# Kernel tuning notes

Measured on AMD Instinct MI355X. Metric: run time of the kernel, lower is better.

## Reference

```python
import jax, jax.numpy as jnp
import numpy as np

N = 40000      # nodes
E = 640000     # edges (avg degree 16)
F_IN = 32      # input node feature dim
G = 64         # graphs in batch
DIMS = [(F_IN, 128), (128, 64), (64, 32), (32, 16)]


def setup_inputs() -> dict:
    key = jax.random.key(0)
    ks = jax.random.split(key, 16)
    inp = {
        "x": jax.random.normal(ks[0], (N, F_IN), jnp.float32),
        "edge_index": jax.random.randint(ks[1], (2, E), 0, N),
        "batch": jnp.sort(jax.random.randint(ks[2], (N,), 0, G)),
    }
    k = 3
    for i, (din, dout) in enumerate(DIMS, 1):
        s = 1.0 / np.sqrt(din)
        inp[f"W{i}_rel"] = jax.random.uniform(ks[k], (din, dout), jnp.float32, -s, s); k += 1
        inp[f"b{i}"] = jax.random.uniform(ks[k], (dout,), jnp.float32, -s, s); k += 1
        inp[f"W{i}_root"] = jax.random.uniform(ks[k], (din, dout), jnp.float32, -s, s); k += 1
    s = 1.0 / np.sqrt(16)
    inp["Wfc"] = jax.random.uniform(ks[15], (16, 1), jnp.float32, -s, s)
    inp["bfc"] = jax.random.uniform(jax.random.fold_in(key, 99), (1,), jnp.float32, -s, s)
    return inp


def _graph_conv(x, src, dst, W_rel, b, W_root):
    # PyG GraphConv (aggr='add'): out_i = (sum_{j->i} x_j) @ W_rel + b + x_i @ W_root
    agg = jax.ops.segment_sum(x[src], dst, num_segments=N)  # gather -> scatter-add
    return agg @ W_rel + b + x @ W_root


def reference(x, edge_index, batch,
              W1_rel, b1, W1_root, W2_rel, b2, W2_root,
              W3_rel, b3, W3_root, W4_rel, b4, W4_root, Wfc, bfc):
    src, dst = edge_index[0], edge_index[1]
    h = jax.nn.relu(_graph_conv(x, src, dst, W1_rel, b1, W1_root))
    h = jax.nn.relu(_graph_conv(h, src, dst, W2_rel, b2, W2_root))
    h = jax.nn.relu(_graph_conv(h, src, dst, W3_rel, b3, W3_root))
    h = _graph_conv(h, src, dst, W4_rel, b4, W4_root)  # no ReLU before pooling
    # global mean pool per graph
    sums = jax.ops.segment_sum(h, batch, num_segments=G)                       # [G, 16]
    counts = jax.ops.segment_sum(jnp.ones((N, 1), h.dtype), batch, num_segments=G)
    pooled = sums / jnp.maximum(counts, 1.0)
    return pooled @ Wfc + bfc  # [G, 1]
```

## Files before the change

kernel.cpp:

```cpp
#include <hip/hip_runtime.h>

#define NN 40000
#define NE 640000
#define NG 64
#define SCAN_NB ((NN + 255) / 256)
#define CCAP 768

__device__ __forceinline__ float fcomp(const float4& v, int t) {
    return t == 0 ? v.x : t == 1 ? v.y : t == 2 ? v.z : v.w;
}
__device__ __forceinline__ unsigned int pack2bf(float a, float b) {
    unsigned int ua = __float_as_uint(a);
    unsigned int ub = __float_as_uint(b);
    ua = (ua + 0x7fffu + ((ua >> 16) & 1u)) >> 16;
    ub = (ub + 0x7fffu + ((ub >> 16) & 1u)) >> 16;
    return ua | (ub << 16);
}
__device__ __forceinline__ uint2 pack4bf(const float4& v) {
    return make_uint2(pack2bf(v.x, v.y), pack2bf(v.z, v.w));
}
__device__ __forceinline__ float lo2f(unsigned int u) { return __uint_as_float(u << 16); }
__device__ __forceinline__ float hi2f(unsigned int u) { return __uint_as_float(u & 0xffff0000u); }
__device__ __forceinline__ void acc8(const uint4& u, float4& lo, float4& hi) {
    lo.x += lo2f(u.x); lo.y += hi2f(u.x); lo.z += lo2f(u.y); lo.w += hi2f(u.y);
    hi.x += lo2f(u.z); hi.y += hi2f(u.z); hi.z += lo2f(u.w); hi.w += hi2f(u.w);
}

__global__ __launch_bounds__(256) void prep_kernel(
        int* __restrict__ zp, int nz,
        const float4* __restrict__ x4,
        uint2* __restrict__ xb,
        const float* __restrict__ W4rel,
        const float* __restrict__ W4root,
        const float* __restrict__ b4,
        const float* __restrict__ Wfc,
        float* __restrict__ wf) {
    int i = blockIdx.x * 256 + threadIdx.x;
    if (i < nz) zp[i] = 0;
    if (i < NN * 8) { float4 v = x4[i]; xb[i] = pack4bf(v); }
    if (blockIdx.x == 0) {
        int t = threadIdx.x;
        if (t < 32) {
            float a = 0.f, b = 0.f;
#pragma unroll
            for (int j = 0; j < 16; ++j) {
                float w = Wfc[j];
                a += W4rel[t * 16 + j] * w;
                b += W4root[t * 16 + j] * w;
            }
            wf[t] = a;
            wf[32 + t] = b;
        } else if (t == 32) {
            float s = 0.f;
#pragma unroll
            for (int j = 0; j < 16; ++j) s += b4[j] * Wfc[j];
            wf[64] = s;
        }
    }
}

__global__ void hist_kernel(const int* __restrict__ dst, int* __restrict__ deg,
                            int* __restrict__ epos) {
    int e = blockIdx.x * blockDim.x + threadIdx.x;
    if (e < NE) epos[e] = atomicAdd(&deg[dst[e]], 1);
}

__global__ __launch_bounds__(256) void scan1_kernel(const int* __restrict__ deg,
                                                    int* __restrict__ rowptr,
                                                    int* __restrict__ bsum) {
    __shared__ int ws[4];
    __shared__ int wpre[4];
    int i = blockIdx.x * 256 + threadIdx.x;
    int lane = threadIdx.x & 63, wid = threadIdx.x >> 6;
    int v = (i < NN) ? deg[i] : 0;
    int incl = v;
#pragma unroll
    for (int off = 1; off < 64; off <<= 1) {
        int u = __shfl_up(incl, off, 64);
        if (lane >= off) incl += u;
    }
    if (lane == 63) ws[wid] = incl;
    __syncthreads();
    if (threadIdx.x == 0) {
        int s = 0;
#pragma unroll
        for (int w = 0; w < 4; ++w) { wpre[w] = s; s += ws[w]; }
        bsum[blockIdx.x] = s;
    }
    __syncthreads();
    if (i < NN) rowptr[i] = wpre[wid] + (incl - v);
}

__global__ __launch_bounds__(256) void scan23_kernel(int* __restrict__ rowptr,
                                                     const int* __restrict__ bsum) {
    __shared__ int ws[4];
    int t = threadIdx.x, b = blockIdx.x;
    int v = (t < b) ? bsum[t] : 0;
#pragma unroll
    for (int off = 32; off; off >>= 1) v += __shfl_xor(v, off, 64);
    if ((t & 63) == 0) ws[t >> 6] = v;
    __syncthreads();
    int soff = ws[0] + ws[1] + ws[2] + ws[3];
    int i = b * 256 + t;
    if (i < NN) rowptr[i] += soff;
    if (b == SCAN_NB - 1 && t == 0) rowptr[NN] = soff + bsum[b];
}

__global__ void fill_kernel(const int* __restrict__ src, const int* __restrict__ dst,
                            const int* __restrict__ rowptr, const int* __restrict__ epos,
                            int* __restrict__ col) {
    int e = blockIdx.x * blockDim.x + threadIdx.x;
    if (e < NE) col[rowptr[dst[e]] + epos[e]] = src[e];
}

__global__ __launch_bounds__(256, 4) void fconv1_kernel(
        const uint4* __restrict__ xb4,
        const float4* __restrict__ x,
        const int* __restrict__ rowptr,
        const int* __restrict__ col,
        const float4* __restrict__ Wrel,
        const float4* __restrict__ Wroot,
        const float4* __restrict__ bias,
        float4* __restrict__ out) {
    __shared__ float4 sA[32][9];
    __shared__ float4 sR[32 * 32];
    __shared__ float4 sT[32 * 32];
    __shared__ int scol[CCAP];
    int t = threadIdx.x;
    for (int i = t; i < 32 * 32; i += 256) { sR[i] = Wrel[i]; sT[i] = Wroot[i]; }
    int blk0 = blockIdx.x * 32;
    int ebeg = rowptr[blk0], eend = rowptr[blk0 + 32];
    bool gat = t < 128;
    int na = t >> 2, c = t & 3;
    int node = blk0 + (gat ? na : 0);
    int beg = gat ? rowptr[node] : 0;
    int end = gat ? rowptr[node + 1] : 0;
    float4 aLo = {0.f, 0.f, 0.f, 0.f}, aHi = {0.f, 0.f, 0.f, 0.f};
    for (int base = ebeg; base < eend; base += CCAP) {
        int cnt = eend - base < CCAP ? eend - base : CCAP;
        __syncthreads();
        for (int i = t; i < cnt; i += 256) scol[i] = col[base + i];
        __syncthreads();
        if (gat) {
            int lo = beg > base ? beg : base;
            int hi = end < base + cnt ? end : base + cnt;
            int e = lo;
            for (; e + 4 <= hi; e += 4) {
                uint4 u0 = xb4[(size_t)scol[e - base] * 4 + c];
                uint4 u1 = xb4[(size_t)scol[e - base + 1] * 4 + c];
                uint4 u2 = xb4[(size_t)scol[e - base + 2] * 4 + c];
                uint4 u3 = xb4[(size_t)scol[e - base + 3] * 4 + c];
                acc8(u0, aLo, aHi); acc8(u1, aLo, aHi);
                acc8(u2, aLo, aHi); acc8(u3, aLo, aHi);
            }
            for (; e < hi; ++e) {
                uint4 u = xb4[(size_t)scol[e - base] * 4 + c];
                acc8(u, aLo, aHi);
            }
        }
    }
    if (gat) { sA[na][2 * c] = aLo; sA[na][2 * c + 1] = aHi; }
    __syncthreads();
    int jg = t % 16, mg = t / 16;
    int n0 = blk0 + mg * 2;
    float4 bb0 = bias[2 * jg], bb1 = bias[2 * jg + 1];
    float4 acc00 = bb0, acc01 = bb1, acc10 = bb0, acc11 = bb1;
#pragma unroll 2
    for (int kc = 0; kc < 8; ++kc) {
        float4 a0 = sA[2 * mg][kc];
        float4 a1 = sA[2 * mg + 1][kc];
        float4 x0 = x[(size_t)n0 * 8 + kc];
        float4 x1 = x[(size_t)(n0 + 1) * 8 + kc];
#pragma unroll
        for (int tt = 0; tt < 4; ++tt) {
            int k = kc * 4 + tt;
            float4 wr0 = sR[k * 32 + 2 * jg], wr1 = sR[k * 32 + 2 * jg + 1];
            float4 wt0 = sT[k * 32 + 2 * jg], wt1 = sT[k * 32 + 2 * jg + 1];
            float av0 = fcomp(a0, tt), xv0 = fcomp(x0, tt);
            float av1 = fcomp(a1, tt), xv1 = fcomp(x1, tt);
            acc00.x += av0 * wr0.x + xv0 * wt0.x;
            acc00.y += av0 * wr0.y + xv0 * wt0.y;
            acc00.z += av0 * wr0.z + xv0 * wt0.z;
            acc00.w += av0 * wr0.w + xv0 * wt0.w;
            acc01.x += av0 * wr1.x + xv0 * wt1.x;
            acc01.y += av0 * wr1.y + xv0 * wt1.y;
            acc01.z += av0 * wr1.z + xv0 * wt1.z;
            acc01.w += av0 * wr1.w + xv0 * wt1.w;
            acc10.x += av1 * wr0.x + xv1 * wt0.x;
            acc10.y += av1 * wr0.y + xv1 * wt0.y;
            acc10.z += av1 * wr0.z + xv1 * wt0.z;
            acc10.w += av1 * wr0.w + xv1 * wt0.w;
            acc11.x += av1 * wr1.x + xv1 * wt1.x;
            acc11.y += av1 * wr1.y + xv1 * wt1.y;
            acc11.z += av1 * wr1.z + xv1 * wt1.z;
            acc11.w += av1 * wr1.w + xv1 * wt1.w;
        }
    }
    float4 r;
    r.x = fmaxf(acc00.x, 0.f); r.y = fmaxf(acc00.y, 0.f);
    r.z = fmaxf(acc00.z, 0.f); r.w = fmaxf(acc00.w, 0.f);
    out[(size_t)n0 * 32 + 2 * jg] = r;
    r.x = fmaxf(acc01.x, 0.f); r.y = fmaxf(acc01.y, 0.f);
    r.z = fmaxf(acc01.z, 0.f); r.w = fmaxf(acc01.w, 0.f);
    out[(size_t)n0 * 32 + 2 * jg + 1] = r;
    r.x = fmaxf(acc10.x, 0.f); r.y = fmaxf(acc10.y, 0.f);
    r.z = fmaxf(acc10.z, 0.f); r.w = fmaxf(acc10.w, 0.f);
    out[(size_t)(n0 + 1) * 32 + 2 * jg] = r;
    r.x = fmaxf(acc11.x, 0.f); r.y = fmaxf(acc11.y, 0.f);
    r.z = fmaxf(acc11.z, 0.f); r.w = fmaxf(acc11.w, 0.f);
    out[(size_t)(n0 + 1) * 32 + 2 * jg + 1] = r;
}

__global__ __launch_bounds__(256, 6) void mmyz_kernel(
        const float4* __restrict__ h,
        const float4* __restrict__ Wrel,
        const float4* __restrict__ Wroot,
        const float4* __restrict__ bias,
        uint2* __restrict__ y2b,
        float4* __restrict__ z2) {
    __shared__ float4 sR[32 * 16];
    __shared__ float4 sT[32 * 16];
    int jl = threadIdx.x % 16;
    int mg = threadIdx.x / 16;
    int n0 = blockIdx.x * 32 + mg * 2;
    float4 bb = bias[jl];
    float4 ay0 = {0.f, 0.f, 0.f, 0.f}, ay1 = {0.f, 0.f, 0.f, 0.f};
    float4 az0 = bb, az1 = bb;
    for (int s = 0; s < 4; ++s) {
        if (s) __syncthreads();
        for (int i = threadIdx.x; i < 512; i += 256) {
            sR[i] = Wrel[s * 512 + i];
            sT[i] = Wroot[s * 512 + i];
        }
        __syncthreads();
#pragma unroll 2
        for (int kc = 0; kc < 8; ++kc) {
            float4 h0 = h[(size_t)n0 * 32 + s * 8 + kc];
            float4 h1 = h[(size_t)(n0 + 1) * 32 + s * 8 + kc];
#pragma unroll
            for (int tt = 0; tt < 4; ++tt) {
                float4 wr = sR[(kc * 4 + tt) * 16 + jl];
                float4 wt = sT[(kc * 4 + tt) * 16 + jl];
                float v0 = fcomp(h0, tt), v1 = fcomp(h1, tt);
                ay0.x += v0 * wr.x; ay0.y += v0 * wr.y;
                ay0.z += v0 * wr.z; ay0.w += v0 * wr.w;
                az0.x += v0 * wt.x; az0.y += v0 * wt.y;
                az0.z += v0 * wt.z; az0.w += v0 * wt.w;
                ay1.x += v1 * wr.x; ay1.y += v1 * wr.y;
                ay1.z += v1 * wr.z; ay1.w += v1 * wr.w;
                az1.x += v1 * wt.x; az1.y += v1 * wt.y;
                az1.z += v1 * wt.z; az1.w += v1 * wt.w;
            }
        }
    }
    y2b[(size_t)n0 * 16 + jl] = pack4bf(ay0);
    z2[(size_t)n0 * 16 + jl] = az0;
    y2b[(size_t)(n0 + 1) * 16 + jl] = pack4bf(ay1);
    z2[(size_t)(n0 + 1) * 16 + jl] = az1;
}

__global__ __launch_bounds__(256, 5) void fconv3_kernel(
        const uint4* __restrict__ yb4,
        const float4* __restrict__ z,
        const int* __restrict__ rowptr,
        const int* __restrict__ col,
        const float4* __restrict__ Wrel,
        const float4* __restrict__ Wroot,
        const float4* __restrict__ bias,
        uint2* __restrict__ y3b,
        float4* __restrict__ z3) {
    __shared__ float4 sH[32][17];
    __shared__ float4 sR[64 * 8];
    __shared__ float4 sT[64 * 8];
    __shared__ int scol[CCAP];
    int t = threadIdx.x;
    for (int i = t; i < 64 * 8; i += 256) { sR[i] = Wrel[i]; sT[i] = Wroot[i]; }
    int blk0 = blockIdx.x * 32;
    int ebeg = rowptr[blk0], eend = rowptr[blk0 + 32];
    int na = t >> 3, c = t & 7;
    int node = blk0 + na;
    int beg = rowptr[node], end = rowptr[node + 1];
    float4 aLo = z[(size_t)node * 16 + 2 * c];
    float4 aHi = z[(size_t)node * 16 + 2 * c + 1];
    for (int base = ebeg; base < eend; base += CCAP) {
        int cnt = eend - base < CCAP ? eend - base : CCAP;
        __syncthreads();
        for (int i = t; i < cnt; i += 256) scol[i] = col[base + i];
        __syncthreads();
        int lo = beg > base ? beg : base;
        int hi = end < base + cnt ? end : base + cnt;
        int e = lo;
        for (; e + 4 <= hi; e += 4) {
            uint4 u0 = yb4[(size_t)scol[e - base] * 8 + c];
            uint4 u1 = yb4[(size_t)scol[e - base + 1] * 8 + c];
            uint4 u2 = yb4[(size_t)scol[e - base + 2] * 8 + c];
            uint4 u3 = yb4[(size_t)scol[e - base + 3] * 8 + c];
            acc8(u0, aLo, aHi); acc8(u1, aLo, aHi);
            acc8(u2, aLo, aHi); acc8(u3, aLo, aHi);
        }
        for (; e < hi; ++e) {
            uint4 u = yb4[(size_t)scol[e - base] * 8 + c];
            acc8(u, aLo, aHi);
        }
    }
    aLo.x = fmaxf(aLo.x, 0.f); aLo.y = fmaxf(aLo.y, 0.f);
    aLo.z = fmaxf(aLo.z, 0.f); aLo.w = fmaxf(aLo.w, 0.f);
    aHi.x = fmaxf(aHi.x, 0.f); aHi.y = fmaxf(aHi.y, 0.f);
    aHi.z = fmaxf(aHi.z, 0.f); aHi.w = fmaxf(aHi.w, 0.f);
    sH[na][2 * c] = aLo;
    sH[na][2 * c + 1] = aHi;
    __syncthreads();
    int jl = t & 7, mg = t >> 3;
    int nodeB = blk0 + mg;
    float4 ay = {0.f, 0.f, 0.f, 0.f};
    float4 az = bias[jl];
#pragma unroll 4
    for (int kc = 0; kc < 16; ++kc) {
        float4 h4 = sH[mg][kc];
#pragma unroll
        for (int tt = 0; tt < 4; ++tt) {
            float hv = fcomp(h4, tt);
            float4 wr = sR[(kc * 4 + tt) * 8 + jl];
            float4 wt = sT[(kc * 4 + tt) * 8 + jl];
            ay.x += hv * wr.x; ay.y += hv * wr.y;
            ay.z += hv * wr.z; ay.w += hv * wr.w;
            az.x += hv * wt.x; az.y += hv * wt.y;
            az.z += hv * wt.z; az.w += hv * wt.w;
        }
    }
    y3b[(size_t)nodeB * 8 + jl] = pack4bf(ay);
    z3[(size_t)nodeB * 8 + jl] = az;
}

__global__ __launch_bounds__(256, 8) void fconv4_kernel(
        const uint4* __restrict__ yb4,
        const float4* __restrict__ z,
        const int* __restrict__ rowptr,
        const int* __restrict__ col,
        const float* __restrict__ wf,
        float* __restrict__ y4,
        float* __restrict__ z4) {
    __shared__ float4 sH[32][9];
    __shared__ float4 sF[8], sRF[8];
    __shared__ float sB;
    __shared__ int scol[CCAP];
    int t = threadIdx.x;
    if (t < 8) sF[t] = ((const float4*)wf)[t];
    else if (t < 16) sRF[t - 8] = ((const float4*)wf)[t];
    else if (t == 16) sB = wf[64];
    int blk0 = blockIdx.x * 32;
    int ebeg = rowptr[blk0], eend = rowptr[blk0 + 32];
    bool gat = t < 128;
    int na = t >> 2, c = t & 3;
    int node = blk0 + (gat ? na : 0);
    int beg = gat ? rowptr[node] : 0;
    int end = gat ? rowptr[node + 1] : 0;
    float4 aLo = {0.f, 0.f, 0.f, 0.f}, aHi = {0.f, 0.f, 0.f, 0.f};
    if (gat) {
        aLo = z[(size_t)node * 8 + 2 * c];
        aHi = z[(size_t)node * 8 + 2 * c + 1];
    }
    for (int base = ebeg; base < eend; base += CCAP) {
        int cnt = eend - base < CCAP ? eend - base : CCAP;
        __syncthreads();
        for (int i = t; i < cnt; i += 256) scol[i] = col[base + i];
        __syncthreads();
        if (gat) {
            int lo = beg > base ? beg : base;
            int hi = end < base + cnt ? end : base + cnt;
            int e = lo;
            for (; e + 4 <= hi; e += 4) {
                uint4 u0 = yb4[(size_t)scol[e - base] * 4 + c];
                uint4 u1 = yb4[(size_t)scol[e - base + 1] * 4 + c];
                uint4 u2 = yb4[(size_t)scol[e - base + 2] * 4 + c];
                uint4 u3 = yb4[(size_t)scol[e - base + 3] * 4 + c];
                acc8(u0, aLo, aHi); acc8(u1, aLo, aHi);
                acc8(u2, aLo, aHi); acc8(u3, aLo, aHi);
            }
            for (; e < hi; ++e) {
                uint4 u = yb4[(size_t)scol[e - base] * 4 + c];
                acc8(u, aLo, aHi);
            }
        }
    }
    if (gat) {
        aLo.x = fmaxf(aLo.x, 0.f); aLo.y = fmaxf(aLo.y, 0.f);
        aLo.z = fmaxf(aLo.z, 0.f); aLo.w = fmaxf(aLo.w, 0.f);
        aHi.x = fmaxf(aHi.x, 0.f); aHi.y = fmaxf(aHi.y, 0.f);
        aHi.z = fmaxf(aHi.z, 0.f); aHi.w = fmaxf(aHi.w, 0.f);
        sH[na][2 * c] = aLo;
        sH[na][2 * c + 1] = aHi;
    }
    __syncthreads();
    if (t < 32) {
        int nd = blk0 + t;
        float ay = 0.f, az = 0.f;
#pragma unroll
        for (int kc = 0; kc < 8; ++kc) {
            float4 h4 = sH[t][kc];
            float4 f = sF[kc], r = sRF[kc];
            ay += h4.x * f.x + h4.y * f.y + h4.z * f.z + h4.w * f.w;
            az += h4.x * r.x + h4.y * r.y + h4.z * r.z + h4.w * r.w;
        }
        y4[nd] = ay;
        z4[nd] = az + sB;
    }
}

__global__ __launch_bounds__(256) void gpool_final_kernel(
        const float* __restrict__ y4,
        const float* __restrict__ z4,
        const int* __restrict__ rowptr,
        const int* __restrict__ col,
        const int* __restrict__ batch,
        float* __restrict__ sums,
        float* __restrict__ counts,
        int* __restrict__ ctr,
        const float* __restrict__ bfc,
        float* __restrict__ out) {
    __shared__ float ls[NG];
    __shared__ float lc[NG];
    __shared__ int sDone;
    if (threadIdx.x < NG) { ls[threadIdx.x] = 0.f; lc[threadIdx.x] = 0.f; }
    if (threadIdx.x == 0) sDone = 0;
    __syncthreads();
    int nd = blockIdx.x * 256 + threadIdx.x;
    if (nd < NN) {
        float v = z4[nd];
        int beg = rowptr[nd], end = rowptr[nd + 1];
        int e = beg;
        for (; e + 4 <= end; e += 4) {
            v += (y4[col[e]] + y4[col[e + 1]]) + (y4[col[e + 2]] + y4[col[e + 3]]);
        }
        for (; e < end; ++e) v += y4[col[e]];
        int g = batch[nd];
        atomicAdd(&ls[g], v);
        atomicAdd(&lc[g], 1.f);
    }
    __syncthreads();
    if (threadIdx.x < NG && lc[threadIdx.x] > 0.f) {
        atomicAdd(&sums[threadIdx.x], ls[threadIdx.x]);
        atomicAdd(&counts[threadIdx.x], lc[threadIdx.x]);
    }
    __threadfence();
    __syncthreads();
    if (threadIdx.x == 0) {
        if (atomicAdd(ctr, 1) == (int)gridDim.x - 1) sDone = 1;
    }
    __syncthreads();
    if (sDone && threadIdx.x < NG) {
        float s = atomicAdd(&sums[threadIdx.x], 0.f);
        float c = atomicAdd(&counts[threadIdx.x], 0.f);
        c = fmaxf(c, 1.0f);
        out[threadIdx.x] = s / c + bfc[0];
    }
}

extern "C" void kernel_launch(void* const* d_in, const int* in_sizes, int n_in,
                              void* d_out, int out_size, void* d_ws, size_t ws_size,
                              hipStream_t stream) {
    const float* x       = (const float*)d_in[0];
    const int*   ei      = (const int*)d_in[1];
    const int*   batch   = (const int*)d_in[2];
    const float* W1_rel  = (const float*)d_in[3];
    const float* b1      = (const float*)d_in[4];
    const float* W1_root = (const float*)d_in[5];
    const float* W2_rel  = (const float*)d_in[6];
    const float* b2      = (const float*)d_in[7];
    const float* W2_root = (const float*)d_in[8];
    const float* W3_rel  = (const float*)d_in[9];
    const float* b3      = (const float*)d_in[10];
    const float* W3_root = (const float*)d_in[11];
    const float* W4_rel  = (const float*)d_in[12];
    const float* b4      = (const float*)d_in[13];
    const float* W4_root = (const float*)d_in[14];
    const float* Wfc     = (const float*)d_in[15];
    const float* bfc     = (const float*)d_in[16];
    float* out = (float*)d_out;

    const int* src = ei;
    const int* dst = ei + NE;

    float* bufH   = (float*)d_ws;
    float* bufZ   = bufH + (size_t)NN * 128;
    float* z3     = bufZ + (size_t)NN * 64;
    float* y4     = z3 + (size_t)NN * 32;
    float* z4     = y4 + NN;
    float* wf     = z4 + NN;
    int*   deg    = (int*)(wf + 68);
    float* sums   = (float*)(deg + NN);
    float* counts = sums + NG;
    int*   ctr    = (int*)(counts + NG);
    int*   rowptr = ctr + 1;
    int*   col    = rowptr + NN + 1;
    int*   bsum   = col + NE;
    int*   epos   = bsum + SCAN_NB + 1;
    uint2* xb     = (uint2*)(epos + NE);
    uint2* y2b    = xb + (size_t)NN * 8;
    uint2* y3b    = y2b + (size_t)NN * 16;

    const int NZ = NN + 2 * NG + 1;

    prep_kernel<<<NN * 8 / 256, 256, 0, stream>>>(
        deg, NZ, (const float4*)x, xb, W4_rel, W4_root, b4, Wfc, wf);

    hist_kernel<<<(NE + 255) / 256, 256, 0, stream>>>(dst, deg, epos);
    scan1_kernel<<<SCAN_NB, 256, 0, stream>>>(deg, rowptr, bsum);
    scan23_kernel<<<SCAN_NB, 256, 0, stream>>>(rowptr, bsum);
    fill_kernel<<<(NE + 255) / 256, 256, 0, stream>>>(src, dst, rowptr, epos, col);

    fconv1_kernel<<<NN / 32, 256, 0, stream>>>(
        (const uint4*)xb, (const float4*)x, rowptr, col,
        (const float4*)W1_rel, (const float4*)W1_root, (const float4*)b1,
        (float4*)bufH);

    mmyz_kernel<<<NN / 32, 256, 0, stream>>>(
        (const float4*)bufH, (const float4*)W2_rel, (const float4*)W2_root,
        (const float4*)b2, y2b, (float4*)bufZ);

    fconv3_kernel<<<NN / 32, 256, 0, stream>>>(
        (const uint4*)y2b, (const float4*)bufZ, rowptr, col,
        (const float4*)W3_rel, (const float4*)W3_root, (const float4*)b3,
        y3b, (float4*)z3);

    fconv4_kernel<<<NN / 32, 256, 0, stream>>>(
        (const uint4*)y3b, (const float4*)z3, rowptr, col, wf, y4, z4);

    gpool_final_kernel<<<(NN + 255) / 256, 256, 0, stream>>>(
        y4, z4, rowptr, col, batch, sums, counts, ctr, bfc, out);
}
```

Before: 154.8 us.

## Fuse layer-1 conv with layer-2 transform and pool directly over edges

Merges the first GraphConv kernel with the layer-2 dense transform. The layer-1 hidden activations stay in shared memory as bf16 rather than being written to and reread from a 40000x128 fp32 global buffer, and one kernel launch is removed. A single shared weight buffer is reused in stages to keep LDS usage in check. The final pooling kernel now walks the edge list with a fixed grid of 320 blocks and does shared-memory atomics per edge, instead of a per-node CSR gather. This adds rounding from bf16 on the hidden state and heavier atomic contention in the pool.

```diff
diff --git a/kernel.cpp b/kernel.cpp
--- a/kernel.cpp
+++ b/kernel.cpp
@@ -5,6 +5,7 @@
 #define NG 64
 #define SCAN_NB ((NN + 255) / 256)
 #define CCAP 768
+#define GPB 320
 
 __device__ __forceinline__ float fcomp(const float4& v, int t) {
     return t == 0 ? v.x : t == 1 ? v.y : t == 2 ? v.z : v.w;
@@ -21,6 +22,9 @@
 }
 __device__ __forceinline__ float lo2f(unsigned int u) { return __uint_as_float(u << 16); }
 __device__ __forceinline__ float hi2f(unsigned int u) { return __uint_as_float(u & 0xffff0000u); }
+__device__ __forceinline__ float4 unp4(const uint2& u) {
+    float4 r; r.x = lo2f(u.x); r.y = hi2f(u.x); r.z = lo2f(u.y); r.w = hi2f(u.y); return r;
+}
 __device__ __forceinline__ void acc8(const uint4& u, float4& lo, float4& hi) {
     lo.x += lo2f(u.x); lo.y += hi2f(u.x); lo.z += lo2f(u.y); lo.w += hi2f(u.y);
     hi.x += lo2f(u.z); hi.y += hi2f(u.z); hi.z += lo2f(u.w); hi.w += hi2f(u.w);
@@ -113,25 +117,28 @@
     if (e < NE) col[rowptr[dst[e]] + epos[e]] = src[e];
 }
 
-__global__ __launch_bounds__(256, 4) void fconv1_kernel(
+__global__ __launch_bounds__(256, 5) void fconv12_kernel(
         const uint4* __restrict__ xb4,
         const float4* __restrict__ x,
         const int* __restrict__ rowptr,
         const int* __restrict__ col,
-        const float4* __restrict__ Wrel,
-        const float4* __restrict__ Wroot,
-        const float4* __restrict__ bias,
-        float4* __restrict__ out) {
+        const float4* __restrict__ W1rel,
+        const float4* __restrict__ W1root,
+        const float4* __restrict__ b1,
+        const float4* __restrict__ W2rel,
+        const float4* __restrict__ W2root,
+        const float4* __restrict__ b2,
+        uint2* __restrict__ y2b,
+        float4* __restrict__ z2) {
     __shared__ float4 sA[32][9];
-    __shared__ float4 sR[32 * 32];
-    __shared__ float4 sT[32 * 32];
+    __shared__ uint2 sHb[32][33];
+    __shared__ float4 wbuf[1024];
     __shared__ int scol[CCAP];
     int t = threadIdx.x;
-    for (int i = t; i < 32 * 32; i += 256) { sR[i] = Wrel[i]; sT[i] = Wroot[i]; }
     int blk0 = blockIdx.x * 32;
     int ebeg = rowptr[blk0], eend = rowptr[blk0 + 32];
     bool gat = t < 128;
-    int na = t >> 2, c = t & 3;
+    int na = t >> 2, c4 = t & 3;
     int node = blk0 + (gat ? na : 0);
     int beg = gat ? rowptr[node] : 0;
     int end = gat ? rowptr[node + 1] : 0;
@@ -146,101 +153,99 @@
             int hi = end < base + cnt ? end : base + cnt;
             int e = lo;
             for (; e + 4 <= hi; e += 4) {
-                uint4 u0 = xb4[(size_t)scol[e - base] * 4 + c];
-                uint4 u1 = xb4[(size_t)scol[e - base + 1] * 4 + c];
-                uint4 u2 = xb4[(size_t)scol[e - base + 2] * 4 + c];
-                uint4 u3 = xb4[(size_t)scol[e - base + 3] * 4 + c];
+                uint4 u0 = xb4[(size_t)scol[e - base] * 4 + c4];
+                uint4 u1 = xb4[(size_t)scol[e - base + 1] * 4 + c4];
+                uint4 u2 = xb4[(size_t)scol[e - base + 2] * 4 + c4];
+                uint4 u3 = xb4[(size_t)scol[e - base + 3] * 4 + c4];
                 acc8(u0, aLo, aHi); acc8(u1, aLo, aHi);
                 acc8(u2, aLo, aHi); acc8(u3, aLo, aHi);
             }
             for (; e < hi; ++e) {
-                uint4 u = xb4[(size_t)scol[e - base] * 4 + c];
+                uint4 u = xb4[(size_t)scol[e - base] * 4 + c4];
                 acc8(u, aLo, aHi);
             }
         }
     }
-    if (gat) { sA[na][2 * c] = aLo; sA[na][2 * c + 1] = aHi; }
+    if (gat) { sA[na][2 * c4] = aLo; sA[na][2 * c4 + 1] = aHi; }
+    __syncthreads();
+    for (int i = t; i < 1024; i += 256) wbuf[i] = W1rel[i];
     __syncthreads();
     int jg = t % 16, mg = t / 16;
     int n0 = blk0 + mg * 2;
-    float4 bb0 = bias[2 * jg], bb1 = bias[2 * jg + 1];
+    float4 bb0 = b1[2 * jg], bb1 = b1[2 * jg + 1];
     float4 acc00 = bb0, acc01 = bb1, acc10 = bb0, acc11 = bb1;
 #pragma unroll 2
     for (int kc = 0; kc < 8; ++kc) {
         float4 a0 = sA[2 * mg][kc];
         float4 a1 = sA[2 * mg + 1][kc];
+#pragma unroll
+        for (int tt = 0; tt < 4; ++tt) {
+            int k = kc * 4 + tt;
+            float4 w0 = wbuf[k * 32 + 2 * jg], w1 = wbuf[k * 32 + 2 * jg + 1];
+            float av0 = fcomp(a0, tt), av1 = fcomp(a1, tt);
+            acc00.x += av0 * w0.x; acc00.y += av0 * w0.y;
+            acc00.z += av0 * w0.z; acc00.w += av0 * w0.w;
+            acc01.x += av0 * w1.x; acc01.y += av0 * w1.y;
+            acc01.z += av0 * w1.z; acc01.w += av0 * w1.w;
+            acc10.x += av1 * w0.x; acc10.y += av1 * w0.y;
+            acc10.z += av1 * w0.z; acc10.w += av1 * w0.w;
+            acc11.x += av1 * w1.x; acc11.y += av1 * w1.y;
+            acc11.z += av1 * w1.z; acc11.w += av1 * w1.w;
+        }
+    }
+    __syncthreads();
+    for (int i = t; i < 1024; i += 256) wbuf[i] = W1root[i];
+    __syncthreads();
+#pragma unroll 2
+    for (int kc = 0; kc < 8; ++kc) {
         float4 x0 = x[(size_t)n0 * 8 + kc];
         float4 x1 = x[(size_t)(n0 + 1) * 8 + kc];
 #pragma unroll
         for (int tt = 0; tt < 4; ++tt) {
             int k = kc * 4 + tt;
-            float4 wr0 = sR[k * 32 + 2 * jg], wr1 = sR[k * 32 + 2 * jg + 1];
-            float4 wt0 = sT[k * 32 + 2 * jg], wt1 = sT[k * 32 + 2 * jg + 1];
-            float av0 = fcomp(a0, tt), xv0 = fcomp(x0, tt);
-            float av1 = fcomp(a1, tt), xv1 = fcomp(x1, tt);
-            acc00.x += av0 * wr0.x + xv0 * wt0.x;
-            acc00.y += av0 * wr0.y + xv0 * wt0.y;
-            acc00.z += av0 * wr0.z + xv0 * wt0.z;
-            acc00.w += av0 * wr0.w + xv0 * wt0.w;
-            acc01.x += av0 * wr1.x + xv0 * wt1.x;
-            acc01.y += av0 * wr1.y + xv0 * wt1.y;
-            acc01.z += av0 * wr1.z + xv0 * wt1.z;
-            acc01.w += av0 * wr1.w + xv0 * wt1.w;
-            acc10.x += av1 * wr0.x + xv1 * wt0.x;
-            acc10.y += av1 * wr0.y + xv1 * wt0.y;
-            acc10.z += av1 * wr0.z + xv1 * wt0.z;
-            acc10.w += av1 * wr0.w + xv1 * wt0.w;
-            acc11.x += av1 * wr1.x + xv1 * wt1.x;
-            acc11.y += av1 * wr1.y + xv1 * wt1.y;
-            acc11.z += av1 * wr1.z + xv1 * wt1.z;
-            acc11.w += av1 * wr1.w + xv1 * wt1.w;
-        }
-    }
-    float4 r;
-    r.x = fmaxf(acc00.x, 0.f); r.y = fmaxf(acc00.y, 0.f);
-    r.z = fmaxf(acc00.z, 0.f); r.w = fmaxf(acc00.w, 0.f);
-    out[(size_t)n0 * 32 + 2 * jg] = r;
-    r.x = fmaxf(acc01.x, 0.f); r.y = fmaxf(acc01.y, 0.f);
-    r.z = fmaxf(acc01.z, 0.f); r.w = fmaxf(acc01.w, 0.f);
-    out[(size_t)n0 * 32 + 2 * jg + 1] = r;
-    r.x = fmaxf(acc10.x, 0.f); r.y = fmaxf(acc10.y, 0.f);
-    r.z = fmaxf(acc10.z, 0.f); r.w = fmaxf(acc10.w, 0.f);
-    out[(size_t)(n0 + 1) * 32 + 2 * jg] = r;
-    r.x = fmaxf(acc11.x, 0.f); r.y = fmaxf(acc11.y, 0.f);
-    r.z = fmaxf(acc11.z, 0.f); r.w = fmaxf(acc11.w, 0.f);
-    out[(size_t)(n0 + 1) * 32 + 2 * jg + 1] = r;
-}
-
-__global__ __launch_bounds__(256, 6) void mmyz_kernel(
-        const float4* __restrict__ h,
-        const float4* __restrict__ Wrel,
-        const float4* __restrict__ Wroot,
-        const float4* __restrict__ bias,
-        uint2* __restrict__ y2b,
-        float4* __restrict__ z2) {
-    __shared__ float4 sR[32 * 16];
-    __shared__ float4 sT[32 * 16];
-    int jl = threadIdx.x % 16;
-    int mg = threadIdx.x / 16;
-    int n0 = blockIdx.x * 32 + mg * 2;
-    float4 bb = bias[jl];
+            float4 w0 = wbuf[k * 32 + 2 * jg], w1 = wbuf[k * 32 + 2 * jg + 1];
+            float xv0 = fcomp(x0, tt), xv1 = fcomp(x1, tt);
+            acc00.x += xv0 * w0.x; acc00.y += xv0 * w0.y;
+            acc00.z += xv0 * w0.z; acc00.w += xv0 * w0.w;
+            acc01.x += xv0 * w1.x; acc01.y += xv0 * w1.y;
+            acc01.z += xv0 * w1.z; acc01.w += xv0 * w1.w;
+            acc10.x += xv1 * w0.x; acc10.y += xv1 * w0.y;
+            acc10.z += xv1 * w0.z; acc10.w += xv1 * w0.w;
+            acc11.x += xv1 * w1.x; acc11.y += xv1 * w1.y;
+            acc11.z += xv1 * w1.z; acc11.w += xv1 * w1.w;
+        }
+    }
+    acc00.x = fmaxf(acc00.x, 0.f); acc00.y = fmaxf(acc00.y, 0.f);
+    acc00.z = fmaxf(acc00.z, 0.f); acc00.w = fmaxf(acc00.w, 0.f);
+    acc01.x = fmaxf(acc01.x, 0.f); acc01.y = fmaxf(acc01.y, 0.f);
+    acc01.z = fmaxf(acc01.z, 0.f); acc01.w = fmaxf(acc01.w, 0.f);
+    acc10.x = fmaxf(acc10.x, 0.f); acc10.y = fmaxf(acc10.y, 0.f);
+    acc10.z = fmaxf(acc10.z, 0.f); acc10.w = fmaxf(acc10.w, 0.f);
+    acc11.x = fmaxf(acc11.x, 0.f); acc11.y = fmaxf(acc11.y, 0.f);
+    acc11.z = fmaxf(acc11.z, 0.f); acc11.w = fmaxf(acc11.w, 0.f);
+    sHb[2 * mg][2 * jg] = pack4bf(acc00);
+    sHb[2 * mg][2 * jg + 1] = pack4bf(acc01);
+    sHb[2 * mg + 1][2 * jg] = pack4bf(acc10);
+    sHb[2 * mg + 1][2 * jg + 1] = pack4bf(acc11);
+    int bna0 = t >> 4, bna1 = bna0 + 16, bc = t & 15;
+    float4 bb = b2[bc];
     float4 ay0 = {0.f, 0.f, 0.f, 0.f}, ay1 = {0.f, 0.f, 0.f, 0.f};
     float4 az0 = bb, az1 = bb;
     for (int s = 0; s < 4; ++s) {
-        if (s) __syncthreads();
-        for (int i = threadIdx.x; i < 512; i += 256) {
-            sR[i] = Wrel[s * 512 + i];
-            sT[i] = Wroot[s * 512 + i];
+        __syncthreads();
+        for (int i = t; i < 512; i += 256) {
+            wbuf[i] = W2rel[s * 512 + i];
+            wbuf[512 + i] = W2root[s * 512 + i];
         }
         __syncthreads();
 #pragma unroll 2
         for (int kc = 0; kc < 8; ++kc) {
-            float4 h0 = h[(size_t)n0 * 32 + s * 8 + kc];
-            float4 h1 = h[(size_t)(n0 + 1) * 32 + s * 8 + kc];
+            float4 h0 = unp4(sHb[bna0][s * 8 + kc]);
+            float4 h1 = unp4(sHb[bna1][s * 8 + kc]);
 #pragma unroll
             for (int tt = 0; tt < 4; ++tt) {
-                float4 wr = sR[(kc * 4 + tt) * 16 + jl];
-                float4 wt = sT[(kc * 4 + tt) * 16 + jl];
+                float4 wr = wbuf[(kc * 4 + tt) * 16 + bc];
+                float4 wt = wbuf[512 + (kc * 4 + tt) * 16 + bc];
                 float v0 = fcomp(h0, tt), v1 = fcomp(h1, tt);
                 ay0.x += v0 * wr.x; ay0.y += v0 * wr.y;
                 ay0.z += v0 * wr.z; ay0.w += v0 * wr.w;
@@ -253,10 +258,11 @@
             }
         }
     }
-    y2b[(size_t)n0 * 16 + jl] = pack4bf(ay0);
-    z2[(size_t)n0 * 16 + jl] = az0;
-    y2b[(size_t)(n0 + 1) * 16 + jl] = pack4bf(ay1);
-    z2[(size_t)(n0 + 1) * 16 + jl] = az1;
+    int nd0 = blk0 + bna0, nd1 = blk0 + bna1;
+    y2b[(size_t)nd0 * 16 + bc] = pack4bf(ay0);
+    z2[(size_t)nd0 * 16 + bc] = az0;
+    y2b[(size_t)nd1 * 16 + bc] = pack4bf(ay1);
+    z2[(size_t)nd1 * 16 + bc] = az1;
 }
 
 __global__ __launch_bounds__(256, 5) void fconv3_kernel(
@@ -407,11 +413,11 @@
     }
 }
 
-__global__ __launch_bounds__(256) void gpool_final_kernel(
+__global__ __launch_bounds__(256) void gpoolE_kernel(
         const float* __restrict__ y4,
         const float* __restrict__ z4,
-        const int* __restrict__ rowptr,
-        const int* __restrict__ col,
+        const int* __restrict__ src,
+        const int* __restrict__ dst,
         const int* __restrict__ batch,
         float* __restrict__ sums,
         float* __restrict__ counts,
@@ -424,21 +430,18 @@
     if (threadIdx.x < NG) { ls[threadIdx.x] = 0.f; lc[threadIdx.x] = 0.f; }
     if (threadIdx.x == 0) sDone = 0;
     __syncthreads();
-    int nd = blockIdx.x * 256 + threadIdx.x;
-    if (nd < NN) {
-        float v = z4[nd];
-        int beg = rowptr[nd], end = rowptr[nd + 1];
-        int e = beg;
-        for (; e + 4 <= end; e += 4) {
-            v += (y4[col[e]] + y4[col[e + 1]]) + (y4[col[e + 2]] + y4[col[e + 3]]);
-        }
-        for (; e < end; ++e) v += y4[col[e]];
-        int g = batch[nd];
-        atomicAdd(&ls[g], v);
+    int gid = blockIdx.x * 256 + threadIdx.x;
+    for (int e = gid; e < NE; e += GPB * 256) {
+        int s = src[e], d = dst[e];
+        atomicAdd(&ls[batch[d]], y4[s]);
+    }
+    for (int n = gid; n < NN; n += GPB * 256) {
+        int g = batch[n];
+        atomicAdd(&ls[g], z4[n]);
         atomicAdd(&lc[g], 1.f);
     }
     __syncthreads();
-    if (threadIdx.x < NG && lc[threadIdx.x] > 0.f) {
+    if (threadIdx.x < NG) {
         atomicAdd(&sums[threadIdx.x], ls[threadIdx.x]);
         atomicAdd(&counts[threadIdx.x], lc[threadIdx.x]);
     }
@@ -481,8 +484,7 @@
     const int* src = ei;
     const int* dst = ei + NE;
 
-    float* bufH   = (float*)d_ws;
-    float* bufZ   = bufH + (size_t)NN * 128;
+    float* bufZ   = (float*)d_ws;
     float* z3     = bufZ + (size_t)NN * 64;
     float* y4     = z3 + (size_t)NN * 32;
     float* z4     = y4 + NN;
@@ -509,14 +511,11 @@
     scan23_kernel<<<SCAN_NB, 256, 0, stream>>>(rowptr, bsum);
     fill_kernel<<<(NE + 255) / 256, 256, 0, stream>>>(src, dst, rowptr, epos, col);
 
-    fconv1_kernel<<<NN / 32, 256, 0, stream>>>(
+    fconv12_kernel<<<NN / 32, 256, 0, stream>>>(
         (const uint4*)xb, (const float4*)x, rowptr, col,
         (const float4*)W1_rel, (const float4*)W1_root, (const float4*)b1,
-        (float4*)bufH);
-
-    mmyz_kernel<<<NN / 32, 256, 0, stream>>>(
-        (const float4*)bufH, (const float4*)W2_rel, (const float4*)W2_root,
-        (const float4*)b2, y2b, (float4*)bufZ);
+        (const float4*)W2_rel, (const float4*)W2_root, (const float4*)b2,
+        y2b, (float4*)bufZ);
 
     fconv3_kernel<<<NN / 32, 256, 0, stream>>>(
         (const uint4*)y2b, (const float4*)bufZ, rowptr, col,
@@ -526,6 +525,6 @@
     fconv4_kernel<<<NN / 32, 256, 0, stream>>>(
         (const uint4*)y3b, (const float4*)z3, rowptr, col, wf, y4, z4);
 
-    gpool_final_kernel<<<(NN + 255) / 256, 256, 0, stream>>>(
-        y4, z4, rowptr, col, batch, sums, counts, ctr, bfc, out);
-}
+    gpoolE_kernel<<<GPB, 256, 0, stream>>>(
+        y4, z4, src, dst, batch, sums, counts, ctr, bfc, out);
+}
```

New measurement: 168.9 us. 9.1% more time.
